# Performance work log

Hardware: AMD Instinct MI355X
Metric: run time of the kernel (lower is better)

## Reference

```python
import jax, jax.numpy as jnp
import numpy as np

B, S, D, H = 4, 2048, 1024, 16
DK = D // H

def setup_inputs() -> dict:
    key = jax.random.key(0)
    ks = jax.random.split(key, 8)
    scale = 1.0 / np.sqrt(D)
    return {
        'q': jax.random.normal(ks[0], (B, S, D), jnp.float32),
        'k': jax.random.normal(ks[1], (B, S, D), jnp.float32),
        'v': jax.random.normal(ks[2], (B, S, D), jnp.float32),
        'Wq': jax.random.normal(ks[3], (D, D), jnp.float32) * scale,
        'bq': jnp.zeros((D,), jnp.float32),
        'Wk': jax.random.normal(ks[4], (D, D), jnp.float32) * scale,
        'bk': jnp.zeros((D,), jnp.float32),
        'Wv': jax.random.normal(ks[5], (D, D), jnp.float32) * scale,
        'bv': jnp.zeros((D,), jnp.float32),
        'Wo': jax.random.normal(ks[6], (D, D), jnp.float32) * scale,
        'bo': jnp.zeros((D,), jnp.float32),
    }

def reference(q, k, v, Wq, bq, Wk, bk, Wv, bv, Wo, bo):
    # Linear projections (torch Linear: x @ W.T + b; here W stored as [in,out])
    qp = q @ Wq + bq  # [B,S,D]
    kp = k @ Wk + bk
    vp = v @ Wv + bv
    # split heads -> [B,H,S,DK]
    qh = qp.reshape(B, S, H, DK).transpose(0, 2, 1, 3)
    kh = kp.reshape(B, S, H, DK).transpose(0, 2, 1, 3)
    vh = vp.reshape(B, S, H, DK).transpose(0, 2, 1, 3)
    scores = jnp.einsum('bhqd,bhkd->bhqk', qh, kh) / jnp.sqrt(jnp.float32(DK))
    attn = jax.nn.softmax(scores, axis=-1)  # [B,H,S,S]
    out = jnp.einsum('bhqk,bhkd->bhqd', attn, vh)
    out = out.transpose(0, 2, 1, 3).reshape(B, S, D)
    return out @ Wo + bo
```

## Files before the change

kernel.cpp:

```cpp
#include <hip/hip_runtime.h>
#include <math.h>

#define SEQ 2048
#define DIM 1024
#define NH 16

typedef short s8v __attribute__((ext_vector_type(8)));
typedef short s4v __attribute__((ext_vector_type(4)));
typedef float f4v __attribute__((ext_vector_type(4)));

__device__ __forceinline__ unsigned short f2bf(float x) {
    unsigned u = __float_as_uint(x);
    u += 0x7FFFu + ((u >> 16) & 1u);
    return (unsigned short)(u >> 16);
}
__device__ __forceinline__ unsigned cvt_pk_bf16(float lo, float hi) {
    unsigned r;
    asm("v_cvt_pk_bf16_f32 %0, %1, %2" : "=v"(r) : "v"(lo), "v"(hi));
    return r;
}

__global__ __launch_bounds__(256)
void conv_all(const float* __restrict__ q, const float* __restrict__ k,
              const float* __restrict__ v,
              unsigned short* __restrict__ qb, unsigned short* __restrict__ kb,
              unsigned short* __restrict__ vb, int n4,
              const float* __restrict__ W0, const float* __restrict__ W1,
              const float* __restrict__ W2, const float* __restrict__ W3,
              unsigned short* __restrict__ T0, unsigned short* __restrict__ T1,
              unsigned short* __restrict__ T2, unsigned short* __restrict__ T3)
{
    __shared__ float T[64][65];
    const int t = threadIdx.x;
    if (blockIdx.y < 3) {
        const float* in = (blockIdx.y == 0) ? q : (blockIdx.y == 1) ? k : v;
        unsigned short* out = (blockIdx.y == 0) ? qb : (blockIdx.y == 1) ? kb : vb;
        int i = blockIdx.x * 256 + t;
        if (i >= n4) return;
        float4 x = ((const float4*)in)[i];
        ushort4 o;
        o.x = f2bf(x.x); o.y = f2bf(x.y); o.z = f2bf(x.z); o.w = f2bf(x.w);
        ((ushort4*)out)[i] = o;
        return;
    }
    int id = blockIdx.x;
    if (id >= 1024) return;
    const int wz = id >> 8, rem = id & 255;
    const int bxx = rem & 15, byy = rem >> 4;
    const float* W = (wz == 0) ? W0 : (wz == 1) ? W1 : (wz == 2) ? W2 : W3;
    unsigned short* WT = (wz == 0) ? T0 : (wz == 1) ? T1 : (wz == 2) ? T2 : T3;
    const int n0 = bxx * 64, k0 = byy * 64;
    #pragma unroll
    for (int i = 0; i < 4; i++) {
        int idx = t + i * 256;
        int r = idx >> 4, c4 = idx & 15;
        float4 vv = *(const float4*)&W[(size_t)(k0 + r) * DIM + n0 + c4 * 4];
        T[r][c4 * 4 + 0] = vv.x; T[r][c4 * 4 + 1] = vv.y;
        T[r][c4 * 4 + 2] = vv.z; T[r][c4 * 4 + 3] = vv.w;
    }
    __syncthreads();
    #pragma unroll
    for (int i = 0; i < 4; i++) {
        int idx = t + i * 256;
        int rn = idx >> 4, c4 = idx & 15;
        ushort4 o;
        o.x = f2bf(T[c4 * 4 + 0][rn]);
        o.y = f2bf(T[c4 * 4 + 1][rn]);
        o.z = f2bf(T[c4 * 4 + 2][rn]);
        o.w = f2bf(T[c4 * 4 + 3][rn]);
        *(ushort4*)&WT[(size_t)(n0 + rn) * DIM + k0 + c4 * 4] = o;
    }
}

template<int MODE>
__device__ __forceinline__
void gemm_core(const unsigned short* __restrict__ A,
               const unsigned short* __restrict__ BT,
               const float* __restrict__ bias, void* __restrict__ outp,
               float scale, int bx, int by)
{
    __shared__ __align__(16) unsigned short smem[17408];
    unsigned short* As = smem;
    unsigned short* Bs = smem + 128 * 64;
    const int t = threadIdx.x;
    const int lane = t & 63, w = t >> 6;
    const int l15 = lane & 15, quad = lane >> 4;
    const int bm = by * 128, bn = bx * 128;
    const int wm = (w & 1) * 64, wn = (w >> 1) * 64;
    const int lrow = lane >> 3, lcol = (lane & 7) * 8;

    f4v acc[4][4];
    #pragma unroll
    for (int mi = 0; mi < 4; mi++)
        #pragma unroll
        for (int ni = 0; ni < 4; ni++)
            acc[mi][ni] = (f4v){0.f, 0.f, 0.f, 0.f};

    for (int k0 = 0; k0 < DIM; k0 += 64) {
        __syncthreads();
        #pragma unroll
        for (int i = 0; i < 4; i++) {
            int ci = w + i * 4;
            int row = ci * 8 + lrow;
            __builtin_amdgcn_global_load_lds(
                (const __attribute__((address_space(1))) unsigned int*)
                    (A + (size_t)(bm + row) * DIM + k0 + lcol),
                (__attribute__((address_space(3))) unsigned int*)(As + ci * 8 * 64),
                16, 0, 0);
            __builtin_amdgcn_global_load_lds(
                (const __attribute__((address_space(1))) unsigned int*)
                    (BT + (size_t)(bn + row) * DIM + k0 + lcol),
                (__attribute__((address_space(3))) unsigned int*)(Bs + ci * 8 * 64),
                16, 0, 0);
        }
        __syncthreads();
        #pragma unroll
        for (int kc = 0; kc < 2; kc++) {
            const int ko = kc * 32 + quad * 8;
            s8v af[4], bf[4];
            #pragma unroll
            for (int mi = 0; mi < 4; mi++)
                af[mi] = *(const s8v*)&As[(wm + mi * 16 + l15) * 64 + ko];
            #pragma unroll
            for (int ni = 0; ni < 4; ni++)
                bf[ni] = *(const s8v*)&Bs[(wn + ni * 16 + l15) * 64 + ko];
            #pragma unroll
            for (int mi = 0; mi < 4; mi++)
                #pragma unroll
                for (int ni = 0; ni < 4; ni++)
                    acc[mi][ni] = __builtin_amdgcn_mfma_f32_16x16x32_bf16(
                        af[mi], bf[ni], acc[mi][ni], 0, 0, 0);
        }
    }

    if (MODE == 0) {
        #pragma unroll
        for (int mi = 0; mi < 4; mi++)
            #pragma unroll
            for (int ni = 0; ni < 4; ni++)
                #pragma unroll
                for (int r = 0; r < 4; r++) {
                    int m = bm + wm + mi * 16 + quad * 4 + r;
                    int n = bn + wn + ni * 16 + l15;
                    ((float*)outp)[(size_t)m * DIM + n] = acc[mi][ni][r] + bias[n];
                }
    } else {
        __syncthreads();
        unsigned short* Cs = smem;
        if (MODE == 1) {
            #pragma unroll
            for (int mi = 0; mi < 4; mi++)
                #pragma unroll
                for (int ni = 0; ni < 4; ni++)
                    #pragma unroll
                    for (int r = 0; r < 4; r++) {
                        int ml = wm + mi * 16 + quad * 4 + r;
                        int nl = wn + ni * 16 + l15;
                        float val = (acc[mi][ni][r] + bias[bn + nl]) * scale;
                        Cs[ml * 136 + nl] = f2bf(val);
                    }
        } else {
            #pragma unroll
            for (int mi = 0; mi < 4; mi++)
                #pragma unroll
                for (int ni = 0; ni < 4; ni++) {
                    int nl = wn + ni * 16 + l15;
                    int m0 = wm + mi * 16 + quad * 4;
                    s4v o;
                    #pragma unroll
                    for (int r = 0; r < 4; r++)
                        o[r] = (short)f2bf(acc[mi][ni][r] + bias[bn + nl]);
                    *(s4v*)&Cs[nl * 136 + m0] = o;
                }
        }
        __syncthreads();
        #pragma unroll
        for (int it = 0; it < 8; it++) {
            int idx = t + it * 256;
            int rr = idx >> 4, cc = (idx & 15) * 8;
            if (MODE == 1) {
                int m = bm + rr, n = bn + cc;
                int b = m >> 11, s = m & (SEQ - 1);
                int h = n >> 6, dk = n & 63;
                *(s8v*)&((unsigned short*)outp)[(((size_t)(b * NH + h)) * SEQ + s) * 64 + dk] =
                    *(const s8v*)&Cs[rr * 136 + cc];
            } else {
                int n = bn + rr, m0 = bm + cc;
                int b = m0 >> 11, s = m0 & (SEQ - 1);
                int h = n >> 6, dk = n & 63;
                *(s8v*)&((unsigned short*)outp)[((size_t)(b * NH + h) * 64 + dk) * SEQ + s] =
                    *(const s8v*)&Cs[rr * 136 + cc];
            }
        }
    }
}

template<int NX, int NWG>
__device__ __forceinline__ void xcd_swizzle(int& bx, int& by) {
    const int lin = by * NX + bx;
    const int lin2 = (lin & 7) * (NWG >> 3) + (lin >> 3);
    bx = lin2 % NX;
    by = lin2 / NX;
}

__global__ __launch_bounds__(256)
void qkv_gemm(const unsigned short* __restrict__ qb, const unsigned short* __restrict__ kb,
              const unsigned short* __restrict__ vb,
              const unsigned short* __restrict__ WqT, const unsigned short* __restrict__ WkT,
              const unsigned short* __restrict__ WvT,
              const float* __restrict__ bq, const float* __restrict__ bk,
              const float* __restrict__ bv,
              unsigned short* __restrict__ qp, unsigned short* __restrict__ kp,
              unsigned short* __restrict__ vpT)
{
    int bx = blockIdx.x, by = blockIdx.y;
    xcd_swizzle<8, 512>(bx, by);
    const int z = blockIdx.z;
    if (z == 0) {
        gemm_core<1>(qb, WqT, bq, qp, 0.18033688011112042f, bx, by);
    } else if (z == 1) {
        gemm_core<1>(kb, WkT, bk, kp, 1.0f, bx, by);
    } else {
        gemm_core<2>(vb, WvT, bv, vpT, 1.0f, bx, by);
    }
}

__global__ __launch_bounds__(256)
void out_gemm(const unsigned short* __restrict__ A, const unsigned short* __restrict__ BT,
              const float* __restrict__ bias, float* __restrict__ outp)
{
    int bx = blockIdx.x, by = blockIdx.y;
    xcd_swizzle<8, 512>(bx, by);
    gemm_core<0>(A, BT, bias, outp, 1.0f, bx, by);
}

__global__ __launch_bounds__(256)
void attn_mfma(const unsigned short* __restrict__ Q,
               const unsigned short* __restrict__ Kp,
               const unsigned short* __restrict__ VT,
               unsigned short* __restrict__ AO)
{
    __shared__ __align__(16) unsigned short Ks[64 * 72];
    __shared__ __align__(16) unsigned short Vs[64 * 72];
    __shared__ __align__(16) unsigned short Ps[4][32 * 72];
    const int t = threadIdx.x;
    const int lane = t & 63, w = t >> 6;
    const int l15 = lane & 15, quad = lane >> 4;

    int bxs = blockIdx.x, bys = blockIdx.y;
    xcd_swizzle<16, 1024>(bxs, bys);
    const int bh = bys, q0 = bxs * 128;

    const unsigned short* qbase = Q + ((size_t)bh * SEQ + q0 + w * 32) * 64;
    const unsigned short* kbase = Kp + (size_t)bh * SEQ * 64;
    const unsigned short* vtbase = VT + (size_t)bh * 64 * SEQ;

    s8v qf[2][2];
    #pragma unroll
    for (int qs = 0; qs < 2; qs++)
        #pragma unroll
        for (int kc = 0; kc < 2; kc++)
            qf[qs][kc] = *(const s8v*)&qbase[(qs * 16 + l15) * 64 + kc * 32 + quad * 8];

    f4v o_acc[2][4];
    #pragma unroll
    for (int qs = 0; qs < 2; qs++)
        #pragma unroll
        for (int df = 0; df < 4; df++) o_acc[qs][df] = (f4v){0.f, 0.f, 0.f, 0.f};
    f4v o_l[2];
    o_l[0] = (f4v){0.f, 0.f, 0.f, 0.f};
    o_l[1] = (f4v){0.f, 0.f, 0.f, 0.f};
    const s8v ones = {0x3F80, 0x3F80, 0x3F80, 0x3F80, 0x3F80, 0x3F80, 0x3F80, 0x3F80};

    const int srow = t >> 3, scol = (t & 7) * 8;
    unsigned short* Pw = (unsigned short*)Ps[w];

    s8v kreg[2], vreg[2];
    #pragma unroll
    for (int i = 0; i < 2; i++) {
        int row = srow + i * 32;
        kreg[i] = *(const s8v*)&kbase[(size_t)row * 64 + scol];
        vreg[i] = *(const s8v*)&vtbase[(size_t)row * SEQ + scol];
    }
    #pragma unroll
    for (int i = 0; i < 2; i++) {
        int row = srow + i * 32;
        *(s8v*)&Ks[row * 72 + scol] = kreg[i];
        *(s8v*)&Vs[row * 72 + scol] = vreg[i];
    }
    __syncthreads();

    for (int kt = 0; kt < 32; kt++) {
        if (kt < 31) {
            #pragma unroll
            for (int i = 0; i < 2; i++) {
                int row = srow + i * 32;
                kreg[i] = *(const s8v*)&kbase[((size_t)((kt + 1) * 64 + row)) * 64 + scol];
                vreg[i] = *(const s8v*)&vtbase[(size_t)row * SEQ + (kt + 1) * 64 + scol];
            }
        }

        f4v s_acc[2][4];
        #pragma unroll
        for (int qs = 0; qs < 2; qs++)
            #pragma unroll
            for (int mf = 0; mf < 4; mf++) s_acc[qs][mf] = (f4v){0.f, 0.f, 0.f, 0.f};
        __builtin_amdgcn_s_setprio(1);
        #pragma unroll
        for (int kc = 0; kc < 2; kc++) {
            const int ko = kc * 32 + quad * 8;
            #pragma unroll
            for (int mf = 0; mf < 4; mf++) {
                s8v kf = *(const s8v*)&Ks[(mf * 16 + l15) * 72 + ko];
                #pragma unroll
                for (int qs = 0; qs < 2; qs++)
                    s_acc[qs][mf] = __builtin_amdgcn_mfma_f32_16x16x32_bf16(
                        kf, qf[qs][kc], s_acc[qs][mf], 0, 0, 0);
            }
        }
        __builtin_amdgcn_s_setprio(0);

        #pragma unroll
        for (int qs = 0; qs < 2; qs++) {
            #pragma unroll
            for (int mf = 0; mf < 4; mf++) {
                float p0 = __builtin_amdgcn_exp2f(s_acc[qs][mf][0]);
                float p1 = __builtin_amdgcn_exp2f(s_acc[qs][mf][1]);
                float p2 = __builtin_amdgcn_exp2f(s_acc[qs][mf][2]);
                float p3 = __builtin_amdgcn_exp2f(s_acc[qs][mf][3]);
                uint2 pk;
                pk.x = cvt_pk_bf16(p0, p1);
                pk.y = cvt_pk_bf16(p2, p3);
                *(s4v*)&Pw[(qs * 16 + l15) * 72 + mf * 16 + quad * 4] =
                    __builtin_bit_cast(s4v, pk);
            }
        }

        asm volatile("" ::: "memory");
        __builtin_amdgcn_sched_barrier(0);

        #pragma unroll
        for (int kc2 = 0; kc2 < 2; kc2++) {
            const int ko = kc2 * 32 + quad * 8;
            s8v pf0 = *(const s8v*)&Pw[(0 * 16 + l15) * 72 + ko];
            s8v pf1 = *(const s8v*)&Pw[(1 * 16 + l15) * 72 + ko];
            __builtin_amdgcn_s_setprio(1);
            o_l[0] = __builtin_amdgcn_mfma_f32_16x16x32_bf16(pf0, ones, o_l[0], 0, 0, 0);
            o_l[1] = __builtin_amdgcn_mfma_f32_16x16x32_bf16(pf1, ones, o_l[1], 0, 0, 0);
            #pragma unroll
            for (int df = 0; df < 4; df++) {
                s8v vf = *(const s8v*)&Vs[(df * 16 + l15) * 72 + ko];
                o_acc[0][df] = __builtin_amdgcn_mfma_f32_16x16x32_bf16(pf0, vf, o_acc[0][df], 0, 0, 0);
                o_acc[1][df] = __builtin_amdgcn_mfma_f32_16x16x32_bf16(pf1, vf, o_acc[1][df], 0, 0, 0);
            }
            __builtin_amdgcn_s_setprio(0);
        }

        __syncthreads();
        if (kt < 31) {
            #pragma unroll
            for (int i = 0; i < 2; i++) {
                int row = srow + i * 32;
                *(s8v*)&Ks[row * 72 + scol] = kreg[i];
                *(s8v*)&Vs[row * 72 + scol] = vreg[i];
            }
        }
        __syncthreads();
    }

    const int b = bh >> 4, h = bh & (NH - 1);
    #pragma unroll
    for (int qs = 0; qs < 2; qs++) {
        #pragma unroll
        for (int r = 0; r < 4; r++) {
            float lq = 1.0f / o_l[qs][r];
            int s = q0 + w * 32 + qs * 16 + quad * 4 + r;
            #pragma unroll
            for (int df = 0; df < 4; df++)
                AO[((size_t)(b * SEQ + s)) * DIM + h * 64 + df * 16 + l15] =
                    f2bf(o_acc[qs][df][r] * lq);
        }
    }
}

extern "C" void kernel_launch(void* const* d_in, const int* in_sizes, int n_in,
                              void* d_out, int out_size, void* d_ws, size_t ws_size,
                              hipStream_t stream) {
    const float* q  = (const float*)d_in[0];
    const float* k  = (const float*)d_in[1];
    const float* v  = (const float*)d_in[2];
    const float* Wq = (const float*)d_in[3];
    const float* bq = (const float*)d_in[4];
    const float* Wk = (const float*)d_in[5];
    const float* bk = (const float*)d_in[6];
    const float* Wv = (const float*)d_in[7];
    const float* bv = (const float*)d_in[8];
    const float* Wo = (const float*)d_in[9];
    const float* bo = (const float*)d_in[10];
    float* out = (float*)d_out;

    const size_t MK = (size_t)4 * SEQ * DIM;
    const size_t WK = (size_t)DIM * DIM;
    unsigned short* wsu = (unsigned short*)d_ws;
    unsigned short* qb  = wsu;
    unsigned short* kb  = qb + MK;
    unsigned short* vb  = kb + MK;
    unsigned short* WqT = vb + MK;
    unsigned short* WkT = WqT + WK;
    unsigned short* WvT = WkT + WK;
    unsigned short* WoT = WvT + WK;
    unsigned short* qp  = WoT + WK;
    unsigned short* kp  = qp + MK;
    unsigned short* vpT = kp + MK;
    unsigned short* ao  = vpT + MK;

    const int n4 = (int)(MK / 4);
    conv_all<<<dim3((n4 + 255) / 256, 4), 256, 0, stream>>>(
        q, k, v, qb, kb, vb, n4, Wq, Wk, Wv, Wo, WqT, WkT, WvT, WoT);

    qkv_gemm<<<dim3(DIM / 128, (4 * SEQ) / 128, 3), 256, 0, stream>>>(
        qb, kb, vb, WqT, WkT, WvT, bq, bk, bv, qp, kp, vpT);

    attn_mfma<<<dim3(SEQ / 128, 4 * NH), 256, 0, stream>>>(qp, kp, vpT, ao);

    out_gemm<<<dim3(DIM / 128, (4 * SEQ) / 128), 256, 0, stream>>>(ao, WoT, bo, out);
}
```

Before: 365.0 us.

## Software-pipeline attention: overlap next tile QK MFMA with previous exp and PV

Double-buffers the K/V shared-memory tiles and keeps two score accumulator sets so QK^T for tile kt runs alongside the exp and PV for tile kt-1. The loop is unrolled by two and alternates buffers. The aim is to hide exp/convert latency and LDS waits behind independent MFMA work. It costs extra LDS and more live registers, which could reduce occupancy or cause spills.

```diff
diff --git a/kernel.cpp b/kernel.cpp
--- a/kernel.cpp
+++ b/kernel.cpp
@@ -240,8 +240,8 @@
                const unsigned short* __restrict__ VT,
                unsigned short* __restrict__ AO)
 {
-    __shared__ __align__(16) unsigned short Ks[64 * 72];
-    __shared__ __align__(16) unsigned short Vs[64 * 72];
+    __shared__ __align__(16) unsigned short Ks[2][64 * 72];
+    __shared__ __align__(16) unsigned short Vs[2][64 * 72];
     __shared__ __align__(16) unsigned short Ps[4][32 * 72];
     const int t = threadIdx.x;
     const int lane = t & 63, w = t >> 6;
@@ -276,58 +276,36 @@
     unsigned short* Pw = (unsigned short*)Ps[w];
 
     s8v kreg[2], vreg[2];
-    #pragma unroll
-    for (int i = 0; i < 2; i++) {
-        int row = srow + i * 32;
-        kreg[i] = *(const s8v*)&kbase[(size_t)row * 64 + scol];
-        vreg[i] = *(const s8v*)&vtbase[(size_t)row * SEQ + scol];
-    }
-    #pragma unroll
-    for (int i = 0; i < 2; i++) {
-        int row = srow + i * 32;
-        *(s8v*)&Ks[row * 72 + scol] = kreg[i];
-        *(s8v*)&Vs[row * 72 + scol] = vreg[i];
-    }
-    __syncthreads();
-
-    for (int kt = 0; kt < 32; kt++) {
-        if (kt < 31) {
-            #pragma unroll
-            for (int i = 0; i < 2; i++) {
-                int row = srow + i * 32;
-                kreg[i] = *(const s8v*)&kbase[((size_t)((kt + 1) * 64 + row)) * 64 + scol];
-                vreg[i] = *(const s8v*)&vtbase[(size_t)row * SEQ + (kt + 1) * 64 + scol];
-            }
-        }
-
-        f4v s_acc[2][4];
+    f4v sA[2][4], sB[2][4];
+
+    auto qk_into = [&](int kt, int bufc, f4v (&scur)[2][4]) {
         #pragma unroll
         for (int qs = 0; qs < 2; qs++)
             #pragma unroll
-            for (int mf = 0; mf < 4; mf++) s_acc[qs][mf] = (f4v){0.f, 0.f, 0.f, 0.f};
+            for (int mf = 0; mf < 4; mf++) scur[qs][mf] = (f4v){0.f, 0.f, 0.f, 0.f};
         __builtin_amdgcn_s_setprio(1);
         #pragma unroll
         for (int kc = 0; kc < 2; kc++) {
             const int ko = kc * 32 + quad * 8;
             #pragma unroll
             for (int mf = 0; mf < 4; mf++) {
-                s8v kf = *(const s8v*)&Ks[(mf * 16 + l15) * 72 + ko];
-                #pragma unroll
-                for (int qs = 0; qs < 2; qs++)
-                    s_acc[qs][mf] = __builtin_amdgcn_mfma_f32_16x16x32_bf16(
-                        kf, qf[qs][kc], s_acc[qs][mf], 0, 0, 0);
+                s8v kf = *(const s8v*)&Ks[bufc][(mf * 16 + l15) * 72 + ko];
+                scur[0][mf] = __builtin_amdgcn_mfma_f32_16x16x32_bf16(kf, qf[0][kc], scur[0][mf], 0, 0, 0);
+                scur[1][mf] = __builtin_amdgcn_mfma_f32_16x16x32_bf16(kf, qf[1][kc], scur[1][mf], 0, 0, 0);
             }
         }
         __builtin_amdgcn_s_setprio(0);
-
+        (void)kt;
+    };
+    auto exp_pv_prev = [&](f4v (&sprev)[2][4], int bufp) {
         #pragma unroll
         for (int qs = 0; qs < 2; qs++) {
             #pragma unroll
             for (int mf = 0; mf < 4; mf++) {
-                float p0 = __builtin_amdgcn_exp2f(s_acc[qs][mf][0]);
-                float p1 = __builtin_amdgcn_exp2f(s_acc[qs][mf][1]);
-                float p2 = __builtin_amdgcn_exp2f(s_acc[qs][mf][2]);
-                float p3 = __builtin_amdgcn_exp2f(s_acc[qs][mf][3]);
+                float p0 = __builtin_amdgcn_exp2f(sprev[qs][mf][0]);
+                float p1 = __builtin_amdgcn_exp2f(sprev[qs][mf][1]);
+                float p2 = __builtin_amdgcn_exp2f(sprev[qs][mf][2]);
+                float p3 = __builtin_amdgcn_exp2f(sprev[qs][mf][3]);
                 uint2 pk;
                 pk.x = cvt_pk_bf16(p0, p1);
                 pk.y = cvt_pk_bf16(p2, p3);
@@ -335,10 +313,8 @@
                     __builtin_bit_cast(s4v, pk);
             }
         }
-
         asm volatile("" ::: "memory");
         __builtin_amdgcn_sched_barrier(0);
-
         #pragma unroll
         for (int kc2 = 0; kc2 < 2; kc2++) {
             const int ko = kc2 * 32 + quad * 8;
@@ -349,24 +325,59 @@
             o_l[1] = __builtin_amdgcn_mfma_f32_16x16x32_bf16(pf1, ones, o_l[1], 0, 0, 0);
             #pragma unroll
             for (int df = 0; df < 4; df++) {
-                s8v vf = *(const s8v*)&Vs[(df * 16 + l15) * 72 + ko];
+                s8v vf = *(const s8v*)&Vs[bufp][(df * 16 + l15) * 72 + ko];
                 o_acc[0][df] = __builtin_amdgcn_mfma_f32_16x16x32_bf16(pf0, vf, o_acc[0][df], 0, 0, 0);
                 o_acc[1][df] = __builtin_amdgcn_mfma_f32_16x16x32_bf16(pf1, vf, o_acc[1][df], 0, 0, 0);
             }
             __builtin_amdgcn_s_setprio(0);
         }
-
-        __syncthreads();
-        if (kt < 31) {
-            #pragma unroll
-            for (int i = 0; i < 2; i++) {
-                int row = srow + i * 32;
-                *(s8v*)&Ks[row * 72 + scol] = kreg[i];
-                *(s8v*)&Vs[row * 72 + scol] = vreg[i];
-            }
-        }
-        __syncthreads();
-    }
+    };
+    auto load_tile = [&](int kt1) {
+        #pragma unroll
+        for (int i = 0; i < 2; i++) {
+            int row = srow + i * 32;
+            kreg[i] = *(const s8v*)&kbase[((size_t)(kt1 * 64 + row)) * 64 + scol];
+            vreg[i] = *(const s8v*)&vtbase[(size_t)row * SEQ + kt1 * 64 + scol];
+        }
+    };
+    auto write_tile = [&](int buf) {
+        #pragma unroll
+        for (int i = 0; i < 2; i++) {
+            int row = srow + i * 32;
+            *(s8v*)&Ks[buf][row * 72 + scol] = kreg[i];
+            *(s8v*)&Vs[buf][row * 72 + scol] = vreg[i];
+        }
+    };
+
+    load_tile(0);
+    write_tile(0);
+    __syncthreads();
+
+    load_tile(1);
+    qk_into(0, 0, sA);
+    __syncthreads();
+    write_tile(1);
+    __syncthreads();
+
+    for (int kt = 1; kt < 31; kt += 2) {
+        load_tile(kt + 1);
+        qk_into(kt, 1, sB);
+        exp_pv_prev(sA, 0);
+        __syncthreads();
+        write_tile(0);
+        __syncthreads();
+
+        load_tile(kt + 2);
+        qk_into(kt + 1, 0, sA);
+        exp_pv_prev(sB, 1);
+        __syncthreads();
+        write_tile(1);
+        __syncthreads();
+    }
+
+    qk_into(31, 1, sB);
+    exp_pv_prev(sA, 0);
+    exp_pv_prev(sB, 1);
 
     const int b = bh >> 4, h = bh & (NH - 1);
     #pragma unroll
```

After: 356.8 us. 1.02x faster.
